# Kernel tuning notes

Hardware: AMD Instinct MI355X
Metric: run time of the kernel (lower is better)

## Reference

```python
import jax, jax.numpy as jnp
import numpy as np

B, T, D_IN, H, K, C = 8, 2048, 512, 384, 8192, 8
N_BLOCKS = 6
EPS = 1e-5


def conv1d(x, w, b, pad, groups=1):
    # x: [B, Cin, T], w: [Cout, Cin//groups, k]
    y = jax.lax.conv_general_dilated(
        x, w, window_strides=(1,), padding=[(pad, pad)],
        dimension_numbers=("NCH", "OIH", "NCH"), feature_group_count=groups)
    return y + b[None, :, None]


def layernorm(x, g, b):
    # normalize over last axis
    m = jnp.mean(x, axis=-1, keepdims=True)
    v = jnp.mean(jnp.square(x - m), axis=-1, keepdims=True)
    return (x - m) * jax.lax.rsqrt(v + EPS) * g + b


def setup_inputs() -> dict:
    key = jax.random.key(0)
    ks = iter(jax.random.split(key, 32))
    s = 0.02
    inp = {
        "x": jax.random.normal(next(ks), (B, T, D_IN), dtype=jnp.float32),
        "enc_w": jax.random.normal(next(ks), (H, D_IN, 7)) * s,
        "enc_b": jnp.zeros((H,)),
        "enc_ln_g": jnp.ones((H,)),
        "enc_ln_b": jnp.zeros((H,)),
        "blk_dw_w": jax.random.normal(next(ks), (N_BLOCKS, H, 1, 7)) * s,
        "blk_dw_b": jnp.zeros((N_BLOCKS, H)),
        "blk_ln_g": jnp.ones((N_BLOCKS, H)),
        "blk_ln_b": jnp.zeros((N_BLOCKS, H)),
        "blk_w1": jax.random.normal(next(ks), (N_BLOCKS, 4 * H, H)) * s,
        "blk_b1": jnp.zeros((N_BLOCKS, 4 * H)),
        "blk_w2": jax.random.normal(next(ks), (N_BLOCKS, H, 4 * H)) * s,
        "blk_b2": jnp.zeros((N_BLOCKS, H)),
        "out_w": jax.random.normal(next(ks), (C, H, 1)) * s,
        "out_b": jnp.zeros((C,)),
        "embeddings": jax.random.normal(next(ks), (K, C)),
    }
    return inp


def encode(x, enc_w, enc_b, enc_ln_g, enc_ln_b, blk_dw_w, blk_dw_b,
           blk_ln_g, blk_ln_b, blk_w1, blk_b1, blk_w2, blk_b2, out_w, out_b):
    h = x.transpose(0, 2, 1)                       # [B, D_IN, T]
    h = conv1d(h, enc_w, enc_b, pad=3)             # [B, H, T]
    h = layernorm(h.transpose(0, 2, 1), enc_ln_g, enc_ln_b).transpose(0, 2, 1)
    for i in range(N_BLOCKS):
        res = h
        h = conv1d(h, blk_dw_w[i], blk_dw_b[i], pad=3, groups=H)  # depthwise
        ht = h.transpose(0, 2, 1)                  # [B, T, H]
        ht = layernorm(ht, blk_ln_g[i], blk_ln_b[i])
        ht = jnp.einsum("bth,fh->btf", ht, blk_w1[i]) + blk_b1[i]
        ht = jax.nn.gelu(ht, approximate=False)    # torch GELU is exact erf
        ht = jnp.einsum("btf,hf->bth", ht, blk_w2[i]) + blk_b2[i]
        h = ht.transpose(0, 2, 1) + res
    z = conv1d(h, out_w, out_b, pad=0)             # [B, C, T]
    return z.transpose(0, 2, 1)                    # [B, T, C]


def reference(x, enc_w, enc_b, enc_ln_g, enc_ln_b, blk_dw_w, blk_dw_b,
              blk_ln_g, blk_ln_b, blk_w1, blk_b1, blk_w2, blk_b2,
              out_w, out_b, embeddings):
    z = encode(x, enc_w, enc_b, enc_ln_g, enc_ln_b, blk_dw_w, blk_dw_b,
               blk_ln_g, blk_ln_b, blk_w1, blk_b1, blk_w2, blk_b2, out_w, out_b)
    flat = z.reshape(-1, C)                        # [B*T, C]
    # squared euclidean distances: same argmin as torch.cdist
    d2 = (jnp.sum(flat * flat, axis=1, keepdims=True)
          - 2.0 * flat @ embeddings.T
          + jnp.sum(embeddings * embeddings, axis=1))  # [B*T, K]
    indices = jnp.argmin(d2, axis=1)               # [B*T], int
    return indices
```

## Files before the change

kernel.cpp:

```cpp
#include <hip/hip_runtime.h>
#include <math.h>

#define T_   2048
#define DIN  512
#define H_   384
#define H4_  1536
#define BT_  16384

typedef _Float16 half_t;
typedef _Float16 f16x8 __attribute__((ext_vector_type(8)));
typedef float f32x4 __attribute__((ext_vector_type(4)));

#define LO_SCALE 2048.0f
#define LO_INV   4.8828125e-4f

__device__ __forceinline__ void lds_barrier() {
    asm volatile("s_waitcnt lgkmcnt(0)\n\ts_barrier" ::: "memory");
}

__device__ __forceinline__ void split2(float v, half_t* hi, half_t* lo) {
    half_t h = (half_t)v;
    *hi = h;
    *lo = (half_t)((v - (float)h) * LO_SCALE);
}

__global__ void k_split(const float* __restrict__ in, half_t* __restrict__ hi,
                        half_t* __restrict__ lo, long n) {
    long i = (long)blockIdx.x * 256 + threadIdx.x;
    if (i >= n) return;
    split2(in[i], hi + i, lo + i);
}

__global__ void k_split_encw(const float* __restrict__ in, half_t* __restrict__ hi,
                             half_t* __restrict__ lo) {
    int idx = blockIdx.x * 256 + threadIdx.x;
    if (idx >= H_ * 3584) return;
    int n = idx / 3584;
    int r = idx % 3584;
    int tap = r >> 9, i = r & 511;
    split2(in[n * 3584 + i * 7 + tap], hi + idx, lo + idx);
}

__global__ void k_ln(const float* __restrict__ in, float* __restrict__ out,
                     const float* __restrict__ g, const float* __restrict__ b) {
    int row = blockIdx.x;
    int lane = threadIdx.x;
    const float* ir = in + (long)row * H_;
    float v[6];
    float s = 0.f;
#pragma unroll
    for (int j = 0; j < 6; ++j) { v[j] = ir[lane + (j << 6)]; s += v[j]; }
#pragma unroll
    for (int o = 32; o > 0; o >>= 1) s += __shfl_down(s, o, 64);
    s = __shfl(s, 0, 64);
    float mean = s * (1.f / 384.f);
    float q = 0.f;
#pragma unroll
    for (int j = 0; j < 6; ++j) { float d = v[j] - mean; q += d * d; }
#pragma unroll
    for (int o = 32; o > 0; o >>= 1) q += __shfl_down(q, o, 64);
    q = __shfl(q, 0, 64);
    float rstd = rsqrtf(q * (1.f / 384.f) + 1e-5f);
    float* orow = out + (long)row * H_;
#pragma unroll
    for (int j = 0; j < 6; ++j) {
        int c = lane + (j << 6);
        orow[c] = (v[j] - mean) * rstd * g[c] + b[c];
    }
}

__global__ __launch_bounds__(256) void k_dwconv_ln(
    const float* __restrict__ h, half_t* __restrict__ oh,
    half_t* __restrict__ ol,
    const float* __restrict__ w, const float* __restrict__ wb,
    const float* __restrict__ g, const float* __restrict__ gb) {
    int row = (blockIdx.x << 2) + (threadIdx.x >> 6);
    int b = row >> 11;
    int t = row & 2047;
    int lane = threadIdx.x & 63;
    const float* hb = h + ((long)b * T_) * H_;
    float v[6];
    float s = 0.f;
#pragma unroll
    for (int j = 0; j < 6; ++j) {
        int c = lane + (j << 6);
        float acc = wb[c];
        const float* wc = w + c * 7;
#pragma unroll
        for (int k = 0; k < 7; ++k) {
            int tt = t + k - 3;
            if ((unsigned)tt < (unsigned)T_)
                acc = fmaf(hb[(long)tt * H_ + c], wc[k], acc);
        }
        v[j] = acc;
        s += acc;
    }
#pragma unroll
    for (int o = 32; o > 0; o >>= 1) s += __shfl_down(s, o, 64);
    s = __shfl(s, 0, 64);
    float mean = s * (1.f / 384.f);
    float q = 0.f;
#pragma unroll
    for (int j = 0; j < 6; ++j) { float d = v[j] - mean; q += d * d; }
#pragma unroll
    for (int o = 32; o > 0; o >>= 1) q += __shfl_down(q, o, 64);
    q = __shfl(q, 0, 64);
    float rstd = rsqrtf(q * (1.f / 384.f) + 1e-5f);
    long ro = (long)row * H_;
#pragma unroll
    for (int j = 0; j < 6; ++j) {
        int c = lane + (j << 6);
        float val = (v[j] - mean) * rstd * g[c] + gb[c];
        split2(val, oh + ro + c, ol + ro + c);
    }
}

template <int MODE>
__global__ __launch_bounds__(256) void k_mgemm64(
    const half_t* __restrict__ Ah, const half_t* __restrict__ Al,
    const half_t* __restrict__ Bh, const half_t* __restrict__ Bl,
    const float* __restrict__ bias, const float* __restrict__ res,
    float* __restrict__ Cf, int N, int K) {
    __shared__ __align__(16) half_t smem[24576];
    const int tid = threadIdx.x;
    const int lane = tid & 63, wid = tid >> 6;
    const int wn = wid << 5;
    const int quad = lane >> 4, l16 = lane & 15;
    const int m0 = blockIdx.x << 6, n0 = blockIdx.y << 7;
    const int ar = tid >> 2;
    const int ak = (tid & 3) << 3;

    long aoff = 0;
    int tt0 = 0, bq = 0;
    if (MODE == 0) {
        bq = m0 >> 11;
        tt0 = (m0 & 2047) + ar - 3;
    } else {
        aoff = (long)(m0 + ar) * K + ak;
    }
    const long boff0 = (long)(n0 + ar) * K + ak;
    const long boff1 = boff0 + (long)64 * K;

    float4 pAh, pAl, pBh0, pBl0, pBh1, pBl1;
    auto loadregs = [&](int k0) {
        if (MODE == 0) {
            int kk = k0 + ak;
            int tap = kk >> 9, ii = kk & 511;
            int ta = tt0 + tap;
            pAh = pAl = make_float4(0.f, 0.f, 0.f, 0.f);
            if ((unsigned)ta < 2048u) {
                long o = ((long)bq * 2048 + ta) * 512 + ii;
                pAh = *(const float4*)(Ah + o);
                pAl = *(const float4*)(Al + o);
            }
        } else {
            pAh = *(const float4*)(Ah + aoff + k0);
            pAl = *(const float4*)(Al + aoff + k0);
        }
        pBh0 = *(const float4*)(Bh + boff0 + k0);
        pBl0 = *(const float4*)(Bl + boff0 + k0);
        pBh1 = *(const float4*)(Bh + boff1 + k0);
        pBl1 = *(const float4*)(Bl + boff1 + k0);
    };
    const int aw = ar * 32 + ((((tid & 3) ^ ar) & 3) << 3);
    auto storebuf = [&](int buf) {
        *(float4*)&smem[buf * 2048 + aw] = pAh;
        *(float4*)&smem[4096 + buf * 2048 + aw] = pAl;
        int b = 8192 + buf * 4096 + aw;
        *(float4*)&smem[b] = pBh0;
        *(float4*)&smem[b + 2048] = pBh1;
        *(float4*)&smem[b + 8192] = pBl0;
        *(float4*)&smem[b + 8192 + 2048] = pBl1;
    };

    f32x4 acc1[4][2] = {};
    f32x4 acc2[4][2] = {};

    loadregs(0);
    storebuf(0);
    const int nIter = K >> 5;
    int cur = 0;
    const int sw = ((quad ^ l16) & 3) << 3;
    for (int it = 0; it < nIter; ++it) {
        if (it + 1 < nIter) loadregs((it + 1) << 5);
        lds_barrier();
        const int ab = cur * 2048 + l16 * 32 + sw;
        const int bb = 8192 + cur * 4096 + (wn + l16) * 32 + sw;
        f16x8 fah[4], fal[4], fgh[2], fgl[2];
#pragma unroll
        for (int f = 0; f < 4; ++f) {
            fah[f] = *(const f16x8*)&smem[ab + f * 512];
            fal[f] = *(const f16x8*)&smem[ab + 4096 + f * 512];
        }
#pragma unroll
        for (int g = 0; g < 2; ++g) {
            fgh[g] = *(const f16x8*)&smem[bb + g * 512];
            fgl[g] = *(const f16x8*)&smem[bb + 8192 + g * 512];
        }
#pragma unroll
        for (int f = 0; f < 4; ++f)
#pragma unroll
            for (int g = 0; g < 2; ++g)
                acc2[f][g] = __builtin_amdgcn_mfma_f32_16x16x32_f16(fah[f], fgl[g], acc2[f][g], 0, 0, 0);
#pragma unroll
        for (int f = 0; f < 4; ++f)
#pragma unroll
            for (int g = 0; g < 2; ++g)
                acc2[f][g] = __builtin_amdgcn_mfma_f32_16x16x32_f16(fal[f], fgh[g], acc2[f][g], 0, 0, 0);
#pragma unroll
        for (int f = 0; f < 4; ++f)
#pragma unroll
            for (int g = 0; g < 2; ++g)
                acc1[f][g] = __builtin_amdgcn_mfma_f32_16x16x32_f16(fah[f], fgh[g], acc1[f][g], 0, 0, 0);
        if (it + 1 < nIter) storebuf(cur ^ 1);
        cur ^= 1;
    }

    float bv[2];
    bv[0] = bias[n0 + wn + l16];
    bv[1] = bias[n0 + wn + 16 + l16];

#pragma unroll
    for (int f = 0; f < 4; ++f)
#pragma unroll
        for (int g = 0; g < 2; ++g)
#pragma unroll
            for (int r = 0; r < 4; ++r) {
                long row = m0 + f * 16 + quad * 4 + r;
                int col = n0 + wn + g * 16 + l16;
                float v = acc1[f][g][r] + acc2[f][g][r] * LO_INV + bv[g];
                long o = row * N + col;
                if (MODE == 2) v += res[o];
                Cf[o] = v;
            }
}

#define APLANE 4096
#define ASL_OFF 8192
#define BSH_OFF 16384
#define BSL_OFF 24576

__global__ __launch_bounds__(512) void k_mgemm1(
    const half_t* __restrict__ Ah, const half_t* __restrict__ Al,
    const half_t* __restrict__ Bh, const half_t* __restrict__ Bl,
    const float* __restrict__ bias,
    half_t* __restrict__ Ch, half_t* __restrict__ Cl, int N, int K) {
    __shared__ __align__(16) half_t smem[32768];
    const int tid = threadIdx.x;
    const int lane = tid & 63, wid = tid >> 6;
    const int wm = (wid >> 2) << 6, wn = (wid & 3) << 5;
    const int quad = lane >> 4, l16 = lane & 15;
    const int m0 = blockIdx.y << 7, n0 = blockIdx.x << 7;
    const int ar = tid >> 2;
    const int ak = (tid & 3) << 3;

    const long aoff = (long)(m0 + ar) * K + ak;
    const long boff = (long)(n0 + ar) * K + ak;

    float4 pAh, pAl, pBh, pBl;
    auto loadregs = [&](int k0) {
        pAh = *(const float4*)(Ah + aoff + k0);
        pAl = *(const float4*)(Al + aoff + k0);
        pBh = *(const float4*)(Bh + boff + k0);
        pBl = *(const float4*)(Bl + boff + k0);
    };
    const int aw = ar * 32 + ((((tid & 3) ^ ar) & 3) << 3);
    auto storebuf = [&](int buf) {
        int a = buf * APLANE + aw;
        *(float4*)&smem[a] = pAh;
        *(float4*)&smem[a + ASL_OFF] = pAl;
        *(float4*)&smem[a + BSH_OFF] = pBh;
        *(float4*)&smem[a + BSL_OFF] = pBl;
    };

    f32x4 acc1[4][2] = {};
    f32x4 acc2[4][2] = {};

    loadregs(0);
    storebuf(0);
    const int nIter = K >> 5;
    int cur = 0;
    const int sw = ((quad ^ l16) & 3) << 3;
    for (int it = 0; it < nIter; ++it) {
        if (it + 1 < nIter) loadregs((it + 1) << 5);
        lds_barrier();
        const int ab = cur * APLANE + (wm + l16) * 32 + sw;
        const int bb = BSH_OFF + cur * APLANE + (wn + l16) * 32 + sw;
        f16x8 fah[4], fal[4], fgh[2], fgl[2];
#pragma unroll
        for (int f = 0; f < 4; ++f) {
            fah[f] = *(const f16x8*)&smem[ab + f * 512];
            fal[f] = *(const f16x8*)&smem[ab + ASL_OFF + f * 512];
        }
#pragma unroll
        for (int g = 0; g < 2; ++g) {
            fgh[g] = *(const f16x8*)&smem[bb + g * 512];
            fgl[g] = *(const f16x8*)&smem[bb + ASL_OFF + g * 512];
        }
#pragma unroll
        for (int f = 0; f < 4; ++f)
#pragma unroll
            for (int g = 0; g < 2; ++g)
                acc2[f][g] = __builtin_amdgcn_mfma_f32_16x16x32_f16(fah[f], fgl[g], acc2[f][g], 0, 0, 0);
#pragma unroll
        for (int f = 0; f < 4; ++f)
#pragma unroll
            for (int g = 0; g < 2; ++g)
                acc2[f][g] = __builtin_amdgcn_mfma_f32_16x16x32_f16(fal[f], fgh[g], acc2[f][g], 0, 0, 0);
#pragma unroll
        for (int f = 0; f < 4; ++f)
#pragma unroll
            for (int g = 0; g < 2; ++g)
                acc1[f][g] = __builtin_amdgcn_mfma_f32_16x16x32_f16(fah[f], fgh[g], acc1[f][g], 0, 0, 0);
        if (it + 1 < nIter) storebuf(cur ^ 1);
        cur ^= 1;
    }

    float bv[2];
    bv[0] = bias[n0 + wn + l16];
    bv[1] = bias[n0 + wn + 16 + l16];

#pragma unroll
    for (int h2 = 0; h2 < 2; ++h2) {
        __syncthreads();
        if (((wid >> 1) & 1) == h2) {
            int cbase = (wid & 1) << 5;
#pragma unroll
            for (int f = 0; f < 4; ++f)
#pragma unroll
                for (int g = 0; g < 2; ++g)
#pragma unroll
                    for (int r = 0; r < 4; ++r) {
                        int rm = wm + f * 16 + quad * 4 + r;
                        int cn = cbase + g * 16 + l16;
                        float v = acc1[f][g][r] + acc2[f][g][r] * LO_INV + bv[g];
                        v = 0.5f * v * (1.0f + erff(v * 0.70710678118654752f));
                        half_t hh = (half_t)v;
                        smem[rm * 72 + cn] = hh;
                        smem[9216 + rm * 72 + cn] = (half_t)((v - (float)hh) * LO_SCALE);
                    }
        }
        __syncthreads();
        int row = tid >> 2, c16 = (tid & 3) << 4;
        long go = (long)(m0 + row) * N + n0 + (h2 << 6) + c16;
        *(float4*)(Ch + go)     = *(const float4*)&smem[row * 72 + c16];
        *(float4*)(Ch + go + 8) = *(const float4*)&smem[row * 72 + c16 + 8];
        *(float4*)(Cl + go)     = *(const float4*)&smem[9216 + row * 72 + c16];
        *(float4*)(Cl + go + 8) = *(const float4*)&smem[9216 + row * 72 + c16 + 8];
    }
}

__global__ __launch_bounds__(256) void k_outconv_argmin(
    const float* __restrict__ h, const float* __restrict__ ow,
    const float* __restrict__ ob, const float* __restrict__ emb,
    int* __restrict__ outIdx) {
    __shared__ float hs[16][H_ + 1];
    __shared__ float zs[16][8];
    __shared__ float es[16 * 516];
    __shared__ float rb[16][16];
    __shared__ int ri[16][16];
    const int tid = threadIdx.x;
    const int row0 = blockIdx.x << 4;

    for (int i = tid; i < 16 * (H_ / 4); i += 256) {
        int r = i / 96;
        int c4 = (i % 96) << 2;
        float4 v = *(const float4*)&h[((long)(row0 + r)) * H_ + c4];
        hs[r][c4] = v.x; hs[r][c4 + 1] = v.y; hs[r][c4 + 2] = v.z; hs[r][c4 + 3] = v.w;
    }
    __syncthreads();

    if (tid < 128) {
        int r = tid & 15, c = tid >> 4;
        float acc = ob[c];
        const float* wc = ow + c * H_;
        for (int j = 0; j < H_; ++j) acc = fmaf(hs[r][j], wc[j], acc);
        zs[r][c] = acc;
    }
    __syncthreads();

    const int r = tid & 15;
    const int sl = tid >> 4;
    float z0 = zs[r][0], z1 = zs[r][1], z2 = zs[r][2], z3 = zs[r][3];
    float z4 = zs[r][4], z5 = zs[r][5], z6 = zs[r][6], z7 = zs[r][7];
    float best = 3.4e38f;
    int bi = 0;

    for (int ch = 0; ch < 8; ++ch) {
        __syncthreads();
        for (int i = tid; i < 2048; i += 256) {
            int e = i >> 1;
            int half = (i & 1) << 2;
            float4 src = *(const float4*)&emb[(((long)(ch << 10)) + e) * 8 + half];
            *(float4*)&es[(e >> 6) * 516 + ((e & 63) << 3) + half] = src;
        }
        __syncthreads();
        const float* ep = es + sl * 516;
        int gbase = (ch << 10) + (sl << 6);
#pragma unroll 4
        for (int j = 0; j < 64; ++j) {
            float4 e0 = *(const float4*)(ep + (j << 3));
            float4 e1 = *(const float4*)(ep + (j << 3) + 4);
            float t, d;
            t = e0.x - z0; d = t * t;
            t = e0.y - z1; d = fmaf(t, t, d);
            t = e0.z - z2; d = fmaf(t, t, d);
            t = e0.w - z3; d = fmaf(t, t, d);
            t = e1.x - z4; d = fmaf(t, t, d);
            t = e1.y - z5; d = fmaf(t, t, d);
            t = e1.z - z6; d = fmaf(t, t, d);
            t = e1.w - z7; d = fmaf(t, t, d);
            if (d < best) { best = d; bi = gbase + j; }
        }
    }
    rb[r][sl] = best;
    ri[r][sl] = bi;
    __syncthreads();
    if (sl == 0) {
        float bb = rb[r][0];
        int bbi = ri[r][0];
#pragma unroll
        for (int s2 = 1; s2 < 16; ++s2) {
            float v = rb[r][s2];
            int i2 = ri[r][s2];
            if (v < bb || (v == bb && i2 < bbi)) { bb = v; bbi = i2; }
        }
        outIdx[row0 + r] = bbi;
    }
}

extern "C" void kernel_launch(void* const* d_in, const int* in_sizes, int n_in,
                              void* d_out, int out_size, void* d_ws, size_t ws_size,
                              hipStream_t stream) {
    const float* x        = (const float*)d_in[0];
    const float* enc_w    = (const float*)d_in[1];
    const float* enc_b    = (const float*)d_in[2];
    const float* enc_ln_g = (const float*)d_in[3];
    const float* enc_ln_b = (const float*)d_in[4];
    const float* blk_dw_w = (const float*)d_in[5];
    const float* blk_dw_b = (const float*)d_in[6];
    const float* blk_ln_g = (const float*)d_in[7];
    const float* blk_ln_b = (const float*)d_in[8];
    const float* blk_w1   = (const float*)d_in[9];
    const float* blk_b1   = (const float*)d_in[10];
    const float* blk_w2   = (const float*)d_in[11];
    const float* blk_b2   = (const float*)d_in[12];
    const float* out_w    = (const float*)d_in[13];
    const float* out_b    = (const float*)d_in[14];
    const float* emb      = (const float*)d_in[15];
    int* out = (int*)d_out;

    char* base = (char*)d_ws;
    float*  h    = (float*)base;
    half_t* tmph = (half_t*)(base + 25165824);
    half_t* tmpl = (half_t*)(base + 37748736);
    half_t* ht4h = (half_t*)(base + 50331648);
    half_t* ht4l = (half_t*)(base + 100663296);
    half_t* ench = (half_t*)(base + 150994944);
    half_t* encl = (half_t*)(base + 153747456);
    half_t* w1h  = (half_t*)(base + 156499968);
    half_t* w1l  = (half_t*)(base + 163577856);
    half_t* w2h  = (half_t*)(base + 170655744);
    half_t* w2l  = (half_t*)(base + 177733632);
    half_t* xh = ht4h;
    half_t* xl = (half_t*)(base + 50331648 + 16777216);

    k_split<<<(8388608 + 255) / 256, 256, 0, stream>>>(x, xh, xl, 8388608L);
    k_split<<<(3538944 + 255) / 256, 256, 0, stream>>>(blk_w1, w1h, w1l, 3538944L);
    k_split<<<(3538944 + 255) / 256, 256, 0, stream>>>(blk_w2, w2h, w2l, 3538944L);
    k_split_encw<<<(H_ * 3584 + 255) / 256, 256, 0, stream>>>(enc_w, ench, encl);

    k_mgemm64<0><<<dim3(256, 3), 256, 0, stream>>>(xh, xl, ench, encl, enc_b,
                                                   nullptr, h, H_, 3584);
    k_ln<<<BT_, 64, 0, stream>>>(h, h, enc_ln_g, enc_ln_b);

    for (int i = 0; i < 6; ++i) {
        k_dwconv_ln<<<BT_ / 4, 256, 0, stream>>>(h, tmph, tmpl, blk_dw_w + i * H_ * 7,
                                                 blk_dw_b + i * H_, blk_ln_g + i * H_,
                                                 blk_ln_b + i * H_);
        k_mgemm1<<<dim3(12, 128), 512, 0, stream>>>(
            tmph, tmpl, w1h + (long)i * 589824, w1l + (long)i * 589824,
            blk_b1 + i * H4_, ht4h, ht4l, H4_, H_);
        k_mgemm64<2><<<dim3(256, 3), 256, 0, stream>>>(
            ht4h, ht4l, w2h + (long)i * 589824, w2l + (long)i * 589824,
            blk_b2 + i * H_, h, h, H_, H4_);
    }

    k_outconv_argmin<<<BT_ / 16, 256, 0, stream>>>(h, out_w, out_b, emb, out);
}
```

Measured before the change: 1.816 ms.

## Deepen GEMM register prefetch, change LDS swizzle, unify FFN-up GEMM into 64-row kernel

The 64-row split-fp16 GEMM now prefetches two k-steps ahead using two register sets, with the loop unrolled by two over the LDS double buffer. The LDS XOR swizzle now uses row>>1 to cut bank conflicts. Occupancy is hinted with launch_bounds(256,3). The separate 128x128 FFN-up kernel is removed and replaced by a MODE 1 variant of the 64x128 kernel with a GELU epilogue staged through LDS, which launches more, smaller blocks. The extra prefetch registers may raise register pressure, and the smaller tiles reuse less data in the wide GEMM.

```diff
diff --git a/kernel.cpp b/kernel.cpp
--- a/kernel.cpp
+++ b/kernel.cpp
@@ -116,11 +116,12 @@
 }
 
 template <int MODE>
-__global__ __launch_bounds__(256) void k_mgemm64(
+__global__ __launch_bounds__(256, 3) void k_mgemm64(
     const half_t* __restrict__ Ah, const half_t* __restrict__ Al,
     const half_t* __restrict__ Bh, const half_t* __restrict__ Bl,
     const float* __restrict__ bias, const float* __restrict__ res,
-    float* __restrict__ Cf, int N, int K) {
+    float* __restrict__ Cf, half_t* __restrict__ Ch, half_t* __restrict__ Cl,
+    int N, int K) {
     __shared__ __align__(16) half_t smem[24576];
     const int tid = threadIdx.x;
     const int lane = tid & 63, wid = tid >> 6;
@@ -141,51 +142,46 @@
     const long boff0 = (long)(n0 + ar) * K + ak;
     const long boff1 = boff0 + (long)64 * K;
 
-    float4 pAh, pAl, pBh0, pBl0, pBh1, pBl1;
-    auto loadregs = [&](int k0) {
+    struct R6 { float4 ah, al, bh0, bl0, bh1, bl1; };
+    R6 r0, r1;
+    auto loadregs = [&](R6& r, int k0) {
         if (MODE == 0) {
             int kk = k0 + ak;
             int tap = kk >> 9, ii = kk & 511;
             int ta = tt0 + tap;
-            pAh = pAl = make_float4(0.f, 0.f, 0.f, 0.f);
+            r.ah = r.al = make_float4(0.f, 0.f, 0.f, 0.f);
             if ((unsigned)ta < 2048u) {
                 long o = ((long)bq * 2048 + ta) * 512 + ii;
-                pAh = *(const float4*)(Ah + o);
-                pAl = *(const float4*)(Al + o);
+                r.ah = *(const float4*)(Ah + o);
+                r.al = *(const float4*)(Al + o);
             }
         } else {
-            pAh = *(const float4*)(Ah + aoff + k0);
-            pAl = *(const float4*)(Al + aoff + k0);
-        }
-        pBh0 = *(const float4*)(Bh + boff0 + k0);
-        pBl0 = *(const float4*)(Bl + boff0 + k0);
-        pBh1 = *(const float4*)(Bh + boff1 + k0);
-        pBl1 = *(const float4*)(Bl + boff1 + k0);
+            r.ah = *(const float4*)(Ah + aoff + k0);
+            r.al = *(const float4*)(Al + aoff + k0);
+        }
+        r.bh0 = *(const float4*)(Bh + boff0 + k0);
+        r.bl0 = *(const float4*)(Bl + boff0 + k0);
+        r.bh1 = *(const float4*)(Bh + boff1 + k0);
+        r.bl1 = *(const float4*)(Bl + boff1 + k0);
     };
-    const int aw = ar * 32 + ((((tid & 3) ^ ar) & 3) << 3);
-    auto storebuf = [&](int buf) {
-        *(float4*)&smem[buf * 2048 + aw] = pAh;
-        *(float4*)&smem[4096 + buf * 2048 + aw] = pAl;
+    const int aw = ar * 32 + ((((tid & 3) ^ (ar >> 1)) & 3) << 3);
+    auto storebuf = [&](const R6& r, int buf) {
+        *(float4*)&smem[buf * 2048 + aw] = r.ah;
+        *(float4*)&smem[4096 + buf * 2048 + aw] = r.al;
         int b = 8192 + buf * 4096 + aw;
-        *(float4*)&smem[b] = pBh0;
-        *(float4*)&smem[b + 2048] = pBh1;
-        *(float4*)&smem[b + 8192] = pBl0;
-        *(float4*)&smem[b + 8192 + 2048] = pBl1;
+        *(float4*)&smem[b] = r.bh0;
+        *(float4*)&smem[b + 2048] = r.bh1;
+        *(float4*)&smem[b + 8192] = r.bl0;
+        *(float4*)&smem[b + 8192 + 2048] = r.bl1;
     };
 
     f32x4 acc1[4][2] = {};
     f32x4 acc2[4][2] = {};
-
-    loadregs(0);
-    storebuf(0);
-    const int nIter = K >> 5;
-    int cur = 0;
-    const int sw = ((quad ^ l16) & 3) << 3;
-    for (int it = 0; it < nIter; ++it) {
-        if (it + 1 < nIter) loadregs((it + 1) << 5);
-        lds_barrier();
-        const int ab = cur * 2048 + l16 * 32 + sw;
-        const int bb = 8192 + cur * 4096 + (wn + l16) * 32 + sw;
+    const int sw = ((quad ^ (l16 >> 1)) & 3) << 3;
+
+    auto compute = [&](int buf) {
+        const int ab = buf * 2048 + l16 * 32 + sw;
+        const int bb = 8192 + buf * 4096 + (wn + l16) * 32 + sw;
         f16x8 fah[4], fal[4], fgh[2], fgl[2];
 #pragma unroll
         for (int f = 0; f < 4; ++f) {
@@ -212,141 +208,69 @@
 #pragma unroll
             for (int g = 0; g < 2; ++g)
                 acc1[f][g] = __builtin_amdgcn_mfma_f32_16x16x32_f16(fah[f], fgh[g], acc1[f][g], 0, 0, 0);
-        if (it + 1 < nIter) storebuf(cur ^ 1);
-        cur ^= 1;
+    };
+
+    const int nIter = K >> 5;
+    loadregs(r0, 0);
+    loadregs(r1, 32);
+    storebuf(r0, 0);
+    if (nIter > 2) loadregs(r0, 64);
+    for (int it = 0; it < nIter; it += 2) {
+        lds_barrier();
+        compute(0);
+        storebuf(r1, 1);
+        if (it + 3 < nIter) loadregs(r1, (it + 3) << 5);
+        lds_barrier();
+        compute(1);
+        if (it + 2 < nIter) {
+            storebuf(r0, 0);
+            if (it + 4 < nIter) loadregs(r0, (it + 4) << 5);
+        }
     }
 
     float bv[2];
     bv[0] = bias[n0 + wn + l16];
     bv[1] = bias[n0 + wn + 16 + l16];
 
-#pragma unroll
-    for (int f = 0; f < 4; ++f)
-#pragma unroll
-        for (int g = 0; g < 2; ++g)
-#pragma unroll
-            for (int r = 0; r < 4; ++r) {
-                long row = m0 + f * 16 + quad * 4 + r;
-                int col = n0 + wn + g * 16 + l16;
-                float v = acc1[f][g][r] + acc2[f][g][r] * LO_INV + bv[g];
-                long o = row * N + col;
-                if (MODE == 2) v += res[o];
-                Cf[o] = v;
-            }
-}
-
-#define APLANE 4096
-#define ASL_OFF 8192
-#define BSH_OFF 16384
-#define BSL_OFF 24576
-
-__global__ __launch_bounds__(512) void k_mgemm1(
-    const half_t* __restrict__ Ah, const half_t* __restrict__ Al,
-    const half_t* __restrict__ Bh, const half_t* __restrict__ Bl,
-    const float* __restrict__ bias,
-    half_t* __restrict__ Ch, half_t* __restrict__ Cl, int N, int K) {
-    __shared__ __align__(16) half_t smem[32768];
-    const int tid = threadIdx.x;
-    const int lane = tid & 63, wid = tid >> 6;
-    const int wm = (wid >> 2) << 6, wn = (wid & 3) << 5;
-    const int quad = lane >> 4, l16 = lane & 15;
-    const int m0 = blockIdx.y << 7, n0 = blockIdx.x << 7;
-    const int ar = tid >> 2;
-    const int ak = (tid & 3) << 3;
-
-    const long aoff = (long)(m0 + ar) * K + ak;
-    const long boff = (long)(n0 + ar) * K + ak;
-
-    float4 pAh, pAl, pBh, pBl;
-    auto loadregs = [&](int k0) {
-        pAh = *(const float4*)(Ah + aoff + k0);
-        pAl = *(const float4*)(Al + aoff + k0);
-        pBh = *(const float4*)(Bh + boff + k0);
-        pBl = *(const float4*)(Bl + boff + k0);
-    };
-    const int aw = ar * 32 + ((((tid & 3) ^ ar) & 3) << 3);
-    auto storebuf = [&](int buf) {
-        int a = buf * APLANE + aw;
-        *(float4*)&smem[a] = pAh;
-        *(float4*)&smem[a + ASL_OFF] = pAl;
-        *(float4*)&smem[a + BSH_OFF] = pBh;
-        *(float4*)&smem[a + BSL_OFF] = pBl;
-    };
-
-    f32x4 acc1[4][2] = {};
-    f32x4 acc2[4][2] = {};
-
-    loadregs(0);
-    storebuf(0);
-    const int nIter = K >> 5;
-    int cur = 0;
-    const int sw = ((quad ^ l16) & 3) << 3;
-    for (int it = 0; it < nIter; ++it) {
-        if (it + 1 < nIter) loadregs((it + 1) << 5);
-        lds_barrier();
-        const int ab = cur * APLANE + (wm + l16) * 32 + sw;
-        const int bb = BSH_OFF + cur * APLANE + (wn + l16) * 32 + sw;
-        f16x8 fah[4], fal[4], fgh[2], fgl[2];
-#pragma unroll
-        for (int f = 0; f < 4; ++f) {
-            fah[f] = *(const f16x8*)&smem[ab + f * 512];
-            fal[f] = *(const f16x8*)&smem[ab + ASL_OFF + f * 512];
-        }
-#pragma unroll
-        for (int g = 0; g < 2; ++g) {
-            fgh[g] = *(const f16x8*)&smem[bb + g * 512];
-            fgl[g] = *(const f16x8*)&smem[bb + ASL_OFF + g * 512];
-        }
+    if (MODE == 1) {
+        __syncthreads();
 #pragma unroll
         for (int f = 0; f < 4; ++f)
 #pragma unroll
             for (int g = 0; g < 2; ++g)
-                acc2[f][g] = __builtin_amdgcn_mfma_f32_16x16x32_f16(fah[f], fgl[g], acc2[f][g], 0, 0, 0);
+#pragma unroll
+                for (int r = 0; r < 4; ++r) {
+                    int rm = f * 16 + quad * 4 + r;
+                    int cn = wn + g * 16 + l16;
+                    float v = acc1[f][g][r] + acc2[f][g][r] * LO_INV + bv[g];
+                    v = 0.5f * v * (1.0f + erff(v * 0.70710678118654752f));
+                    half_t hh = (half_t)v;
+                    smem[rm * 136 + cn] = hh;
+                    smem[8704 + rm * 136 + cn] = (half_t)((v - (float)hh) * LO_SCALE);
+                }
+        __syncthreads();
+        int row = tid >> 2, c0 = (tid & 3) << 5;
+        long go = (long)(m0 + row) * N + n0 + c0;
+        int so = row * 136 + c0;
+#pragma unroll
+        for (int u = 0; u < 4; ++u) {
+            *(float4*)(Ch + go + u * 8) = *(const float4*)&smem[so + u * 8];
+            *(float4*)(Cl + go + u * 8) = *(const float4*)&smem[8704 + so + u * 8];
+        }
+    } else {
 #pragma unroll
         for (int f = 0; f < 4; ++f)
 #pragma unroll
             for (int g = 0; g < 2; ++g)
-                acc2[f][g] = __builtin_amdgcn_mfma_f32_16x16x32_f16(fal[f], fgh[g], acc2[f][g], 0, 0, 0);
-#pragma unroll
-        for (int f = 0; f < 4; ++f)
-#pragma unroll
-            for (int g = 0; g < 2; ++g)
-                acc1[f][g] = __builtin_amdgcn_mfma_f32_16x16x32_f16(fah[f], fgh[g], acc1[f][g], 0, 0, 0);
-        if (it + 1 < nIter) storebuf(cur ^ 1);
-        cur ^= 1;
-    }
-
-    float bv[2];
-    bv[0] = bias[n0 + wn + l16];
-    bv[1] = bias[n0 + wn + 16 + l16];
-
-#pragma unroll
-    for (int h2 = 0; h2 < 2; ++h2) {
-        __syncthreads();
-        if (((wid >> 1) & 1) == h2) {
-            int cbase = (wid & 1) << 5;
-#pragma unroll
-            for (int f = 0; f < 4; ++f)
-#pragma unroll
-                for (int g = 0; g < 2; ++g)
-#pragma unroll
-                    for (int r = 0; r < 4; ++r) {
-                        int rm = wm + f * 16 + quad * 4 + r;
-                        int cn = cbase + g * 16 + l16;
-                        float v = acc1[f][g][r] + acc2[f][g][r] * LO_INV + bv[g];
-                        v = 0.5f * v * (1.0f + erff(v * 0.70710678118654752f));
-                        half_t hh = (half_t)v;
-                        smem[rm * 72 + cn] = hh;
-                        smem[9216 + rm * 72 + cn] = (half_t)((v - (float)hh) * LO_SCALE);
-                    }
-        }
-        __syncthreads();
-        int row = tid >> 2, c16 = (tid & 3) << 4;
-        long go = (long)(m0 + row) * N + n0 + (h2 << 6) + c16;
-        *(float4*)(Ch + go)     = *(const float4*)&smem[row * 72 + c16];
-        *(float4*)(Ch + go + 8) = *(const float4*)&smem[row * 72 + c16 + 8];
-        *(float4*)(Cl + go)     = *(const float4*)&smem[9216 + row * 72 + c16];
-        *(float4*)(Cl + go + 8) = *(const float4*)&smem[9216 + row * 72 + c16 + 8];
+#pragma unroll
+                for (int r = 0; r < 4; ++r) {
+                    long row = m0 + f * 16 + quad * 4 + r;
+                    int col = n0 + wn + g * 16 + l16;
+                    float v = acc1[f][g][r] + acc2[f][g][r] * LO_INV + bv[g];
+                    long o = row * N + col;
+                    if (MODE == 2) v += res[o];
+                    Cf[o] = v;
+                }
     }
 }
 
@@ -471,19 +395,20 @@
     k_split_encw<<<(H_ * 3584 + 255) / 256, 256, 0, stream>>>(enc_w, ench, encl);
 
     k_mgemm64<0><<<dim3(256, 3), 256, 0, stream>>>(xh, xl, ench, encl, enc_b,
-                                                   nullptr, h, H_, 3584);
+                                                   nullptr, h, nullptr, nullptr,
+                                                   H_, 3584);
     k_ln<<<BT_, 64, 0, stream>>>(h, h, enc_ln_g, enc_ln_b);
 
     for (int i = 0; i < 6; ++i) {
         k_dwconv_ln<<<BT_ / 4, 256, 0, stream>>>(h, tmph, tmpl, blk_dw_w + i * H_ * 7,
                                                  blk_dw_b + i * H_, blk_ln_g + i * H_,
                                                  blk_ln_b + i * H_);
-        k_mgemm1<<<dim3(12, 128), 512, 0, stream>>>(
+        k_mgemm64<1><<<dim3(256, 12), 256, 0, stream>>>(
             tmph, tmpl, w1h + (long)i * 589824, w1l + (long)i * 589824,
-            blk_b1 + i * H4_, ht4h, ht4l, H4_, H_);
+            blk_b1 + i * H4_, nullptr, nullptr, ht4h, ht4l, H4_, H_);
         k_mgemm64<2><<<dim3(256, 3), 256, 0, stream>>>(
             ht4h, ht4l, w2h + (long)i * 589824, w2l + (long)i * 589824,
-            blk_b2 + i * H_, h, h, H_, H4_);
+            blk_b2 + i * H_, h, h, nullptr, nullptr, H_, H4_);
     }
 
     k_outconv_argmin<<<BT_ / 16, 256, 0, stream>>>(h, out_w, out_b, emb, out);
```

New measurement: 4.210 ms. 2.32x slower.
